# Optimization experiments

Measured on AMD Instinct MI355X. Metric: run time of the kernel, lower is better.

Reference implementation:

```python
import jax, jax.numpy as jnp
import numpy as np
from jax import lax

DIM = 384
HEADS = 8
DIM_HEAD = 64
INNER = HEADS * DIM_HEAD  # 512
K = 3
B, H, W = 8, 56, 56
EPS = 1e-5
SCALE = DIM_HEAD ** -0.5


def _dw_proj(x, w_dw, bn_g, bn_b, bn_m, bn_v, w_pw):
    """DepthWiseConv2d: depthwise kxk conv (groups=C_in) -> BatchNorm (inference) -> 1x1 conv."""
    c_in = x.shape[1]
    y = lax.conv_general_dilated(
        x, w_dw, window_strides=(1, 1), padding='SAME',
        feature_group_count=c_in,
        dimension_numbers=('NCHW', 'OIHW', 'NCHW'))
    inv = bn_g / jnp.sqrt(bn_v + EPS)
    y = y * inv[None, :, None, None] + (bn_b - bn_m * inv)[None, :, None, None]
    # 1x1 conv as einsum over channels
    return jnp.einsum('bchw,oc->bohw', y, w_pw)


def _split_heads(t):
    # b (h d) x y -> (b h) (x y) d
    b, _, hh, ww = t.shape
    t = t.reshape(b, HEADS, DIM_HEAD, hh * ww)
    return t.transpose(0, 1, 3, 2).reshape(b * HEADS, hh * ww, DIM_HEAD)


def setup_inputs() -> dict:
    key = jax.random.key(0)
    ks = jax.random.split(key, 12)
    inp = {
        'x': jax.random.normal(ks[0], (B, DIM, H, W), jnp.float32),
        'wq_dw': jax.random.normal(ks[1], (DIM, 1, K, K), jnp.float32) * 0.1,
        'wq_bn_g': jax.random.normal(ks[2], (DIM,), jnp.float32) * 0.1 + 1.0,
        'wq_bn_b': jax.random.normal(ks[3], (DIM,), jnp.float32) * 0.1,
        'wq_bn_m': jax.random.normal(ks[4], (DIM,), jnp.float32) * 0.1,
        'wq_bn_v': jax.random.uniform(ks[5], (DIM,), jnp.float32, 0.5, 1.5),
        'wq_pw': jax.random.normal(ks[6], (INNER, DIM), jnp.float32) * (DIM ** -0.5),
        'wkv_dw': jax.random.normal(ks[7], (DIM, 1, K, K), jnp.float32) * 0.1,
        'wkv_bn_g': jax.random.normal(ks[8], (DIM,), jnp.float32) * 0.1 + 1.0,
        'wkv_bn_b': jax.random.normal(ks[9], (DIM,), jnp.float32) * 0.1,
        'wkv_bn_m': jax.random.normal(ks[10], (DIM,), jnp.float32) * 0.1,
        'wkv_bn_v': jax.random.uniform(ks[11], (DIM,), jnp.float32, 0.5, 1.5),
    }
    k2 = jax.random.split(jax.random.fold_in(key, 1), 3)
    inp['wkv_pw'] = jax.random.normal(k2[0], (2 * INNER, DIM), jnp.float32) * (DIM ** -0.5)
    inp['wo'] = jax.random.normal(k2[1], (DIM, INNER), jnp.float32) * (INNER ** -0.5)
    inp['bo'] = jax.random.normal(k2[2], (DIM,), jnp.float32) * 0.01
    return inp


def reference(x, wq_dw, wq_bn_g, wq_bn_b, wq_bn_m, wq_bn_v, wq_pw,
              wkv_dw, wkv_bn_g, wkv_bn_b, wkv_bn_m, wkv_bn_v, wkv_pw, wo, bo):
    b, _, hh, ww = x.shape
    q = _dw_proj(x, wq_dw, wq_bn_g, wq_bn_b, wq_bn_m, wq_bn_v, wq_pw)
    kv = _dw_proj(x, wkv_dw, wkv_bn_g, wkv_bn_b, wkv_bn_m, wkv_bn_v, wkv_pw)
    k, v = kv[:, :INNER], kv[:, INNER:]
    q, k, v = _split_heads(q), _split_heads(k), _split_heads(v)  # (b*h, N, d)

    # Original math: M0 = diag((q*k).sum(-1))*s; M1+M2 = s*q@k^T;
    # out = M0.sum()*v + (M1 - M0)@v + M2@v = M0.sum()*v + s*q@(k^T@v) - diag*v
    diag = (q * k).sum(-1) * SCALE              # (bh, N)
    m0_sum = diag.sum()                          # global scalar
    ktv = jnp.einsum('bnd,bne->bde', k, v)       # (bh, d, d) -- O(N d^2)
    out = m0_sum * v + SCALE * jnp.einsum('bnd,bde->bne', q, ktv) - diag[..., None] * v

    # (b h) (x y) d -> b (h d) x y
    out = out.reshape(b, HEADS, hh * ww, DIM_HEAD).transpose(0, 1, 3, 2)
    out = out.reshape(b, INNER, hh, ww)
    # to_out: 1x1 conv with bias (dropout p=0)
    return jnp.einsum('bchw,oc->bohw', out, wo) + bo[None, :, None, None]
```

## Files before the change

kernel.cpp:

```cpp
#include <hip/hip_runtime.h>

typedef unsigned short u16;

#define N_SP   3136
#define BNCOL  25088
#define NDIM   384
#define NINNER 512
#define SCALE_F 0.125f

typedef __attribute__((ext_vector_type(8))) short bf16x8;
typedef __attribute__((ext_vector_type(4))) float f32x4;

#define AS1 __attribute__((address_space(1)))
#define AS3 __attribute__((address_space(3)))

__device__ __forceinline__ float bf2f(u16 u) {
  union { unsigned int i; float f; } v; v.i = ((unsigned int)u) << 16; return v.f;
}
__device__ __forceinline__ u16 f2bf(float f) {
  union { float f; unsigned int i; } v; v.f = f;
  unsigned int r = v.i + 0x7fffu + ((v.i >> 16) & 1u);
  return (u16)(r >> 16);
}

__device__ __forceinline__ void g2l16(const u16* g, u16* l) {
  __builtin_amdgcn_global_load_lds((const AS1 unsigned int*)g,
                                   (AS3 unsigned int*)l, 16, 0, 0);
}

__global__ __launch_bounds__(256) void cvt_kernel(
    const float* __restrict__ a, const float* __restrict__ b, const float* __restrict__ c,
    u16* __restrict__ oa, u16* __restrict__ ob, u16* __restrict__ oc,
    const float* __restrict__ qdw, const float* __restrict__ qg, const float* __restrict__ qb2,
    const float* __restrict__ qm,  const float* __restrict__ qv,
    const float* __restrict__ kdw, const float* __restrict__ kg, const float* __restrict__ kb2,
    const float* __restrict__ km,  const float* __restrict__ kvv,
    float* __restrict__ fused)
{
  int i = blockIdx.x * 256 + threadIdx.x;
  if (i < 196608) oa[i] = f2bf(a[i]);
  ob[i] = f2bf(b[i]);
  if (i < 196608) oc[i] = f2bf(c[i]);
  if (i < NDIM) {
    float invq = qg[i] * rsqrtf(qv[i] + 1e-5f);
    float invk = kg[i] * rsqrtf(kvv[i] + 1e-5f);
    float* f = fused + i * 20;
#pragma unroll
    for (int j = 0; j < 9; ++j) { f[j] = qdw[i*9+j] * invq; f[10+j] = kdw[i*9+j] * invk; }
    f[9]  = qb2[i] - qm[i] * invq;
    f[19] = kb2[i] - km[i] * invk;
  }
}

__global__ __launch_bounds__(256) void dwbn_kernel(
    const float* __restrict__ x, const float* __restrict__ fused,
    u16* __restrict__ yq, u16* __restrict__ ykv)
{
  __shared__ u16 Lq[64][40];
  __shared__ u16 Lk[64][40];
  int tid = threadIdx.x;
  int bb = blockIdx.z, c0 = blockIdx.y * 32, p0 = blockIdx.x * 64;
  int pl = tid & 63;
  int cg = __builtin_amdgcn_readfirstlane(tid >> 6);
  int p = p0 + pl;
  int h = p / 56, w = p - h * 56;
  int roff[3], coff[3];
  float mr[3], mc[3];
#pragma unroll
  for (int d = 0; d < 3; ++d) {
    int r = h + d - 1;
    bool vr = (r >= 0) && (r < 56);
    roff[d] = (vr ? r : h) * 56;
    mr[d] = vr ? 1.f : 0.f;
    int cc = w + d - 1;
    bool vc = (cc >= 0) && (cc < 56);
    coff[d] = vc ? cc : w;
    mc[d] = vc ? 1.f : 0.f;
  }
  float m9[9];
#pragma unroll
  for (int dh = 0; dh < 3; ++dh)
#pragma unroll
    for (int dw = 0; dw < 3; ++dw) m9[dh*3+dw] = mr[dh] * mc[dw];

  __attribute__((aligned(16))) u16 oq[8], ok[8];
#pragma unroll
  for (int i = 0; i < 8; ++i) {
    int c = c0 + cg * 8 + i;
    const float* xp = x + ((size_t)bb * NDIM + c) * N_SP;
    const float* f = fused + c * 20;
    float v[9];
#pragma unroll
    for (int dh = 0; dh < 3; ++dh)
#pragma unroll
      for (int dw = 0; dw < 3; ++dw)
        v[dh*3+dw] = xp[roff[dh] + coff[dw]];
    float sq = f[9], sk = f[19];
#pragma unroll
    for (int j = 0; j < 9; ++j) {
      float xm = v[j] * m9[j];
      sq += xm * f[j];
      sk += xm * f[10+j];
    }
    oq[i] = f2bf(sq); ok[i] = f2bf(sk);
  }
  *(ushort4*)&Lq[pl][cg * 8]     = *(ushort4*)&oq[0];
  *(ushort4*)&Lq[pl][cg * 8 + 4] = *(ushort4*)&oq[4];
  *(ushort4*)&Lk[pl][cg * 8]     = *(ushort4*)&ok[0];
  *(ushort4*)&Lk[pl][cg * 8 + 4] = *(ushort4*)&ok[4];
  __syncthreads();
  int pr = tid >> 2, cc2 = (tid & 3) * 8;
  size_t g = ((size_t)bb * N_SP + p0 + pr) * NDIM + c0 + cc2;
  *(ushort4*)(yq + g)      = *(ushort4*)&Lq[pr][cc2];
  *(ushort4*)(yq + g + 4)  = *(ushort4*)&Lq[pr][cc2 + 4];
  *(ushort4*)(ykv + g)     = *(ushort4*)&Lk[pr][cc2];
  *(ushort4*)(ykv + g + 4) = *(ushort4*)&Lk[pr][cc2 + 4];
}

struct GemmLds {
  union {
    struct { u16 A[128 * 32]; u16 B[128 * 32]; } s;
    u16 T[64 * 132];
  } u;
};

__device__ __forceinline__ void gemm_body(GemmLds& lds, int bid,
    const u16* __restrict__ A, const u16* __restrict__ B, int Kd,
    u16* __restrict__ Cout, int Cstride,
    int mode, const float* __restrict__ bias, float* __restrict__ Out, int Mt, int Nt)
{
  int mt, nt;
  if (Nt == 8) {
    int low = bid & 7;
    nt = (bid >> 3) & 7;
    mt = (bid >> 6) * 8 + low;
    if (mt >= Mt) return;
  } else {
    int r = bid & 7, g = bid >> 3;
    mt = g % Mt; nt = (g / Mt) * 8 + r;
    if (nt >= Nt) return;
  }
  int m0 = mt * 128, n0 = nt * 128;

  int tid = threadIdx.x;
  int lane = tid & 63, wv = tid >> 6;
  int wm = (wv >> 1) * 64, wn = (wv & 1) * 64;
  int srow = lane >> 2;
  int sch = (lane & 3) * 8;
  int arow0 = wv * 32;
  const u16* Ag = A + (size_t)(m0 + arow0 + srow) * Kd + sch;
  const u16* Bg = B + (size_t)(n0 + arow0 + srow) * Kd + sch;
  u16* Al = &lds.u.s.A[arow0 * 32];
  u16* Bl = &lds.u.s.B[arow0 * 32];
  f32x4 acc[4][4];
#pragma unroll
  for (int i = 0; i < 4; ++i)
#pragma unroll
    for (int j = 0; j < 4; ++j) acc[i][j] = (f32x4){0.f, 0.f, 0.f, 0.f};

  int ml = lane & 15, q8 = (lane >> 4) * 8;
  for (int k0 = 0; k0 < Kd; k0 += 32) {
    g2l16(Ag + k0, Al);
    g2l16(Ag + k0 + (size_t)16 * Kd, Al + 16 * 32);
    g2l16(Bg + k0, Bl);
    g2l16(Bg + k0 + (size_t)16 * Kd, Bl + 16 * 32);
    __syncthreads();
    bf16x8 af[4], bfr[4];
#pragma unroll
    for (int i = 0; i < 4; ++i) {
      af[i]  = *(const bf16x8*)&lds.u.s.A[(wm + i * 16 + ml) * 32 + q8];
      bfr[i] = *(const bf16x8*)&lds.u.s.B[(wn + i * 16 + ml) * 32 + q8];
    }
#pragma unroll
    for (int i = 0; i < 4; ++i)
#pragma unroll
      for (int j = 0; j < 4; ++j)
        acc[i][j] = __builtin_amdgcn_mfma_f32_16x16x32_bf16(af[i], bfr[j], acc[i][j], 0, 0, 0);
    __syncthreads();
  }

  if (mode == 0) {
    int q4 = (lane >> 4) * 4;
#pragma unroll
    for (int ph = 0; ph < 2; ++ph) {
      if (ph) __syncthreads();
      if ((wv & 1) == ph) {
#pragma unroll
        for (int i = 0; i < 4; ++i)
#pragma unroll
          for (int j = 0; j < 4; ++j) {
            int nl = j * 16 + ml;
            int m = wm + i * 16 + q4;
            ushort4 o;
            o.x = f2bf(acc[i][j][0]); o.y = f2bf(acc[i][j][1]);
            o.z = f2bf(acc[i][j][2]); o.w = f2bf(acc[i][j][3]);
            *(ushort4*)&lds.u.T[nl * 132 + m] = o;
          }
      }
      __syncthreads();
#pragma unroll
      for (int it = 0; it < 4; ++it) {
        int nl = it * 16 + (tid >> 4);
        int mc = (tid & 15) * 8;
        ushort4 a = *(ushort4*)&lds.u.T[nl * 132 + mc];
        ushort4 b = *(ushort4*)&lds.u.T[nl * 132 + mc + 4];
        u16* gp = Cout + (size_t)(n0 + ph * 64 + nl) * Cstride + m0 + mc;
        *(ushort4*)gp = a;
        *(ushort4*)(gp + 4) = b;
      }
    }
  } else {
    int q4 = (lane >> 4) * 4;
#pragma unroll
    for (int i = 0; i < 4; ++i)
#pragma unroll
      for (int j = 0; j < 4; ++j) {
        int n = n0 + wn + j * 16 + ml;
        int bb = n / N_SP, p = n - bb * N_SP;
#pragma unroll
        for (int rr = 0; rr < 4; ++rr) {
          int m = m0 + wm + i * 16 + q4 + rr;
          Out[((size_t)bb * NDIM + m) * N_SP + p] = acc[i][j][rr] + bias[m];
        }
      }
  }
}

__global__ __launch_bounds__(256) void mfma_gemm(
    const u16* __restrict__ A, const u16* __restrict__ B, int Kd,
    u16* __restrict__ Cout, int Cstride,
    int mode, const float* __restrict__ bias, float* __restrict__ Out, int Mt, int Nt)
{
  __shared__ GemmLds lds;
  gemm_body(lds, blockIdx.x, A, B, Kd, Cout, Cstride, mode, bias, Out, Mt, Nt);
}

__global__ __launch_bounds__(256) void mfma_gemm_qkv(
    const u16* __restrict__ Wq, const u16* __restrict__ yq, u16* __restrict__ Qb,
    const u16* __restrict__ ykv, const u16* __restrict__ Wkv, u16* __restrict__ KVb)
{
  __shared__ GemmLds lds;
  int bid = blockIdx.x;
  if (bid < 800)
    gemm_body(lds, bid, Wq, yq, NDIM, Qb, NINNER, 0, nullptr, nullptr, 4, 196);
  else
    gemm_body(lds, bid - 800, ykv, Wkv, NDIM, KVb, BNCOL, 0, nullptr, nullptr, 196, 8);
}

__global__ __launch_bounds__(256) void diag_ktv_kernel(
    const u16* __restrict__ Q, const u16* __restrict__ KV,
    float* __restrict__ dg, float* __restrict__ m0, float* __restrict__ ktv)
{
  __shared__ float wsum[4];
  int bid = blockIdx.x, tid = threadIdx.x;
  if (bid < 448) {
    int bh = bid / 7, xb = bid - bh * 7;
    int bb = bh >> 3, hh = bh & 7;
    int w = tid >> 6, lane = tid & 63;
    int ml = lane & 15, quad = lane >> 4, q8 = quad * 8;
    size_t colbase = (size_t)bb * N_SP + xb * 448 + q8;
    const u16* Ar = KV + (size_t)(hh * 64 + w * 16 + ml) * BNCOL + colbase;
    const u16* Br = KV + (size_t)(NINNER + hh * 64 + ml) * BNCOL + colbase;
    f32x4 acc[4];
#pragma unroll
    for (int j = 0; j < 4; ++j) acc[j] = (f32x4){0.f, 0.f, 0.f, 0.f};
#pragma unroll
    for (int t = 0; t < 14; ++t) {
      int po = t * 32;
      bf16x8 a = *(const bf16x8*)(Ar + po);
#pragma unroll
      for (int j = 0; j < 4; ++j) {
        bf16x8 b = *(const bf16x8*)(Br + (size_t)j * 16 * BNCOL + po);
        acc[j] = __builtin_amdgcn_mfma_f32_16x16x32_bf16(a, b, acc[j], 0, 0, 0);
      }
    }
    float* kt = ktv + bh * 4096;
#pragma unroll
    for (int j = 0; j < 4; ++j)
#pragma unroll
      for (int r = 0; r < 4; ++r)
        atomicAdd(&kt[(w * 16 + quad * 4 + r) * 64 + j * 16 + ml], acc[j][r]);
  } else {
    int b2 = bid - 448;
    int hh = b2 / 98, xb = b2 - hh * 98;
    int bn = xb * 256 + tid;
    const u16* qrow = Q + (size_t)bn * NINNER + hh * 64;
    const u16* kcol = KV + (size_t)(hh * 64) * BNCOL + bn;
    float s = 0.f;
#pragma unroll
    for (int d0 = 0; d0 < 64; d0 += 8) {
      ushort4 a = *(const ushort4*)(qrow + d0);
      ushort4 b = *(const ushort4*)(qrow + d0 + 4);
      const u16* kp = kcol + (size_t)d0 * BNCOL;
      s += bf2f(a.x) * bf2f(kp[0]);
      s += bf2f(a.y) * bf2f(kp[(size_t)1 * BNCOL]);
      s += bf2f(a.z) * bf2f(kp[(size_t)2 * BNCOL]);
      s += bf2f(a.w) * bf2f(kp[(size_t)3 * BNCOL]);
      s += bf2f(b.x) * bf2f(kp[(size_t)4 * BNCOL]);
      s += bf2f(b.y) * bf2f(kp[(size_t)5 * BNCOL]);
      s += bf2f(b.z) * bf2f(kp[(size_t)6 * BNCOL]);
      s += bf2f(b.w) * bf2f(kp[(size_t)7 * BNCOL]);
    }
    s *= SCALE_F;
    dg[(size_t)hh * BNCOL + bn] = s;
    float r = s;
#pragma unroll
    for (int off = 32; off > 0; off >>= 1) r += __shfl_down(r, off);
    if ((tid & 63) == 0) wsum[tid >> 6] = r;
    __syncthreads();
    if (tid == 0) atomicAdd(m0, wsum[0] + wsum[1] + wsum[2] + wsum[3]);
  }
}

__global__ __launch_bounds__(256) void attn_out_kernel(
    const u16* __restrict__ Q, const u16* __restrict__ KV,
    const float* __restrict__ dg, const float* __restrict__ ktv,
    const float* __restrict__ m0p, u16* __restrict__ OutA)
{
  __shared__ u16 Bt[64][72];
  __shared__ u16 T2[64][72];
  __shared__ float ds2[64];
  int bh = blockIdx.y, bb = bh >> 3, hh = bh & 7;
  int p0 = blockIdx.x * 64;
  int tid = threadIdx.x;
  const float* kt = ktv + bh * 4096;
  for (int l = tid; l < 4096; l += 256) {
    int d = l >> 6, e = l & 63;
    Bt[e][d] = f2bf(kt[l]);
  }
  if (tid < 64) ds2[tid] = dg[(size_t)hh * BNCOL + bb * N_SP + p0 + tid];
  __syncthreads();
  int w = tid >> 6, lane = tid & 63;
  int ml = lane & 15, quad = lane >> 4, q8 = quad * 8;
  const u16* Ar = Q + ((size_t)bb * N_SP + p0 + w * 16 + ml) * NINNER + hh * 64 + q8;
  bf16x8 a0 = *(const bf16x8*)Ar;
  bf16x8 a1 = *(const bf16x8*)(Ar + 32);
  f32x4 acc[4];
#pragma unroll
  for (int j = 0; j < 4; ++j) acc[j] = (f32x4){0.f, 0.f, 0.f, 0.f};
#pragma unroll
  for (int j = 0; j < 4; ++j) {
    bf16x8 b0 = *(const bf16x8*)&Bt[j * 16 + ml][q8];
    bf16x8 b1 = *(const bf16x8*)&Bt[j * 16 + ml][32 + q8];
    acc[j] = __builtin_amdgcn_mfma_f32_16x16x32_bf16(a0, b0, acc[j], 0, 0, 0);
    acc[j] = __builtin_amdgcn_mfma_f32_16x16x32_bf16(a1, b1, acc[j], 0, 0, 0);
  }
  float m0v = *m0p;
  size_t pcol = (size_t)bb * N_SP + p0 + w * 16 + quad * 4;
#pragma unroll
  for (int j = 0; j < 4; ++j) {
    const u16* vr = KV + (size_t)(NINNER + hh * 64 + j * 16 + ml) * BNCOL + pcol;
    ushort4 vv = *(const ushort4*)vr;
    const u16* vp = (const u16*)&vv;
#pragma unroll
    for (int r = 0; r < 4; ++r) {
      float dvm = m0v - ds2[w * 16 + quad * 4 + r];
      float o = SCALE_F * acc[j][r] + dvm * bf2f(vp[r]);
      T2[w * 16 + quad * 4 + r][j * 16 + ml] = f2bf(o);
    }
  }
  __syncthreads();
  int pl = tid >> 2, ec = (tid & 3) * 16;
  u16* gp = OutA + ((size_t)bb * N_SP + p0 + pl) * NINNER + hh * 64 + ec;
  *(ushort4*)gp        = *(ushort4*)&T2[pl][ec];
  *(ushort4*)(gp + 4)  = *(ushort4*)&T2[pl][ec + 4];
  *(ushort4*)(gp + 8)  = *(ushort4*)&T2[pl][ec + 8];
  *(ushort4*)(gp + 12) = *(ushort4*)&T2[pl][ec + 12];
}

extern "C" void kernel_launch(void* const* d_in, const int* in_sizes, int n_in,
                              void* d_out, int out_size, void* d_ws, size_t ws_size,
                              hipStream_t stream)
{
  (void)in_sizes; (void)n_in; (void)out_size; (void)ws_size;
  const float* x      = (const float*)d_in[0];
  const float* wq_dw  = (const float*)d_in[1];
  const float* wq_g   = (const float*)d_in[2];
  const float* wq_b   = (const float*)d_in[3];
  const float* wq_m   = (const float*)d_in[4];
  const float* wq_v   = (const float*)d_in[5];
  const float* wq_pw  = (const float*)d_in[6];
  const float* wkv_dw = (const float*)d_in[7];
  const float* wkv_g  = (const float*)d_in[8];
  const float* wkv_b  = (const float*)d_in[9];
  const float* wkv_m  = (const float*)d_in[10];
  const float* wkv_v  = (const float*)d_in[11];
  const float* wkv_pw = (const float*)d_in[12];
  const float* wo     = (const float*)d_in[13];
  const float* bo     = (const float*)d_in[14];
  float* out = (float*)d_out;

  char* ws = (char*)d_ws;
  size_t off = 0;
  auto alloc = [&](size_t bytes) {
    void* p = ws + off; off = (off + bytes + 255) & ~(size_t)255; return p;
  };
  u16* yq   = (u16*)alloc((size_t)BNCOL * NDIM * 2);
  u16* ykv  = (u16*)alloc((size_t)BNCOL * NDIM * 2);
  u16* Qb   = (u16*)alloc((size_t)BNCOL * NINNER * 2);
  u16* KVb  = (u16*)alloc((size_t)2 * NINNER * BNCOL * 2);
  float* dgb  = (float*)alloc((size_t)BNCOL * 8 * 4);
  float* ktvb = (float*)alloc((size_t)64 * 4096 * 4 + 64);
  u16* Wq  = (u16*)alloc((size_t)NINNER * NDIM * 2);
  u16* Wkv = (u16*)alloc((size_t)2 * NINNER * NDIM * 2);
  u16* Wo  = (u16*)alloc((size_t)NDIM * NINNER * 2);
  float* fused = (float*)alloc((size_t)NDIM * 20 * 4);
  float* m0 = ktvb + 64 * 4096;
  u16* OutA = yq;

  hipMemsetAsync(ktvb, 0, (size_t)64 * 4096 * 4 + 4, stream);

  cvt_kernel<<<1536, 256, 0, stream>>>(wq_pw, wkv_pw, wo, Wq, Wkv, Wo,
                                       wq_dw, wq_g, wq_b, wq_m, wq_v,
                                       wkv_dw, wkv_g, wkv_b, wkv_m, wkv_v, fused);

  dwbn_kernel<<<dim3(49, 12, 8), 256, 0, stream>>>(x, fused, yq, ykv);

  mfma_gemm_qkv<<<dim3(800 + 1600), 256, 0, stream>>>(Wq, yq, Qb, ykv, Wkv, KVb);

  diag_ktv_kernel<<<dim3(448 + 784), 256, 0, stream>>>(Qb, KVb, dgb, m0, ktvb);

  attn_out_kernel<<<dim3(49, 64), 256, 0, stream>>>(Qb, KVb, dgb, ktvb, m0, OutA);

  mfma_gemm<<<dim3(3 * 200), 256, 0, stream>>>(Wo, OutA, NINNER, nullptr, 0, 1, bo, out, 3, 196);
}
```

Measured before the change: 299.0 us.

## Double-buffer GEMM LDS tiles and XOR-swizzle chunks to avoid bank conflicts

The GEMM main loop now uses two LDS stages, so the next K-tile's global-to-LDS copy is issued before the MFMAs on the current tile run. This removes one barrier per iteration and overlaps memory latency with compute. It also XOR-swizzles the 8-element chunk index on both the store and load sides to reduce LDS bank conflicts. The cost is double the LDS footprint for A/B tiles (32KB), which may reduce occupancy.

```diff
diff --git a/kernel.cpp b/kernel.cpp
--- a/kernel.cpp
+++ b/kernel.cpp
@@ -119,7 +119,7 @@
 
 struct GemmLds {
   union {
-    struct { u16 A[128 * 32]; u16 B[128 * 32]; } s;
+    u16 buf[2][2][128 * 32];
     u16 T[64 * 132];
   } u;
 };
@@ -146,37 +146,55 @@
   int lane = tid & 63, wv = tid >> 6;
   int wm = (wv >> 1) * 64, wn = (wv & 1) * 64;
   int srow = lane >> 2;
-  int sch = (lane & 3) * 8;
+  int sch = (((lane & 3) ^ ((srow >> 1) & 3))) * 8;
   int arow0 = wv * 32;
   const u16* Ag = A + (size_t)(m0 + arow0 + srow) * Kd + sch;
   const u16* Bg = B + (size_t)(n0 + arow0 + srow) * Kd + sch;
-  u16* Al = &lds.u.s.A[arow0 * 32];
-  u16* Bl = &lds.u.s.B[arow0 * 32];
+
+  int ml = lane & 15;
+  int ch = (((lane >> 4) ^ ((ml >> 1) & 3))) * 8;
+
   f32x4 acc[4][4];
 #pragma unroll
   for (int i = 0; i < 4; ++i)
 #pragma unroll
     for (int j = 0; j < 4; ++j) acc[i][j] = (f32x4){0.f, 0.f, 0.f, 0.f};
 
-  int ml = lane & 15, q8 = (lane >> 4) * 8;
-  for (int k0 = 0; k0 < Kd; k0 += 32) {
+  const int nT = Kd >> 5;
+
+  auto stage = [&](int t, int s) {
+    int k0 = t * 32;
+    u16* Al = &lds.u.buf[s][0][arow0 * 32];
+    u16* Bl = &lds.u.buf[s][1][arow0 * 32];
     g2l16(Ag + k0, Al);
     g2l16(Ag + k0 + (size_t)16 * Kd, Al + 16 * 32);
     g2l16(Bg + k0, Bl);
     g2l16(Bg + k0 + (size_t)16 * Kd, Bl + 16 * 32);
-    __syncthreads();
+  };
+  auto compute = [&](int s) {
+    const u16* As = lds.u.buf[s][0];
+    const u16* Bs = lds.u.buf[s][1];
     bf16x8 af[4], bfr[4];
 #pragma unroll
     for (int i = 0; i < 4; ++i) {
-      af[i]  = *(const bf16x8*)&lds.u.s.A[(wm + i * 16 + ml) * 32 + q8];
-      bfr[i] = *(const bf16x8*)&lds.u.s.B[(wn + i * 16 + ml) * 32 + q8];
+      af[i]  = *(const bf16x8*)&As[(wm + i * 16 + ml) * 32 + ch];
+      bfr[i] = *(const bf16x8*)&Bs[(wn + i * 16 + ml) * 32 + ch];
     }
 #pragma unroll
     for (int i = 0; i < 4; ++i)
 #pragma unroll
       for (int j = 0; j < 4; ++j)
         acc[i][j] = __builtin_amdgcn_mfma_f32_16x16x32_bf16(af[i], bfr[j], acc[i][j], 0, 0, 0);
+  };
+
+  stage(0, 0);
+  __syncthreads();
+  int cur = 0;
+  for (int t = 0; t < nT; ++t) {
+    if (t + 1 < nT) stage(t + 1, cur ^ 1);
+    compute(cur);
     __syncthreads();
+    cur ^= 1;
   }
 
   if (mode == 0) {
```

After: 277.4 us. -7.2%, faster.

## Load GEMM fragments directly from global into registers with double buffering

Applied to the files above, without the earlier changes.

Replaces the LDS-staged global_load_lds tiles in the MFMA GEMM with direct per-lane global loads of bf16x8 fragments, double-buffered across two K-steps of 32, and removes the per-iteration barriers. It also adds a min-blocks hint of 2 to the launch bounds. The goal is to cut LDS traffic and sync stalls. The cost is that each wave now loads its own fragments without sharing through LDS, so global/L2 traffic doubles and the row-strided loads are less coalesced. Register pressure also rises.

```diff
diff --git a/kernel.cpp b/kernel.cpp
--- a/kernel.cpp
+++ b/kernel.cpp
@@ -21,11 +21,6 @@
   union { float f; unsigned int i; } v; v.f = f;
   unsigned int r = v.i + 0x7fffu + ((v.i >> 16) & 1u);
   return (u16)(r >> 16);
-}
-
-__device__ __forceinline__ void g2l16(const u16* g, u16* l) {
-  __builtin_amdgcn_global_load_lds((const AS1 unsigned int*)g,
-                                   (AS3 unsigned int*)l, 16, 0, 0);
 }
 
 __global__ __launch_bounds__(256) void cvt_kernel(
@@ -117,12 +112,7 @@
   *(ushort4*)(ykv + g + 4) = *(ushort4*)&Lk[pr][cc2 + 4];
 }
 
-struct GemmLds {
-  union {
-    struct { u16 A[128 * 32]; u16 B[128 * 32]; } s;
-    u16 T[64 * 132];
-  } u;
-};
+struct GemmLds { u16 T[64 * 132]; };
 
 __device__ __forceinline__ void gemm_body(GemmLds& lds, int bid,
     const u16* __restrict__ A, const u16* __restrict__ B, int Kd,
@@ -145,38 +135,46 @@
   int tid = threadIdx.x;
   int lane = tid & 63, wv = tid >> 6;
   int wm = (wv >> 1) * 64, wn = (wv & 1) * 64;
-  int srow = lane >> 2;
-  int sch = (lane & 3) * 8;
-  int arow0 = wv * 32;
-  const u16* Ag = A + (size_t)(m0 + arow0 + srow) * Kd + sch;
-  const u16* Bg = B + (size_t)(n0 + arow0 + srow) * Kd + sch;
-  u16* Al = &lds.u.s.A[arow0 * 32];
-  u16* Bl = &lds.u.s.B[arow0 * 32];
+  int ml = lane & 15, q8 = (lane >> 4) * 8;
+
+  const u16* Ar = A + (size_t)(m0 + wm + ml) * Kd + q8;
+  const u16* Br = B + (size_t)(n0 + wn + ml) * Kd + q8;
+
   f32x4 acc[4][4];
 #pragma unroll
   for (int i = 0; i < 4; ++i)
 #pragma unroll
     for (int j = 0; j < 4; ++j) acc[i][j] = (f32x4){0.f, 0.f, 0.f, 0.f};
 
-  int ml = lane & 15, q8 = (lane >> 4) * 8;
-  for (int k0 = 0; k0 < Kd; k0 += 32) {
-    g2l16(Ag + k0, Al);
-    g2l16(Ag + k0 + (size_t)16 * Kd, Al + 16 * 32);
-    g2l16(Bg + k0, Bl);
-    g2l16(Bg + k0 + (size_t)16 * Kd, Bl + 16 * 32);
-    __syncthreads();
-    bf16x8 af[4], bfr[4];
+  bf16x8 a0[4], b0[4], a1[4], b1[4];
+#pragma unroll
+  for (int i = 0; i < 4; ++i) {
+    a0[i] = *(const bf16x8*)(Ar + (size_t)(i * 16) * Kd);
+    b0[i] = *(const bf16x8*)(Br + (size_t)(i * 16) * Kd);
+  }
+  for (int k0 = 0; k0 < Kd; k0 += 64) {
 #pragma unroll
     for (int i = 0; i < 4; ++i) {
-      af[i]  = *(const bf16x8*)&lds.u.s.A[(wm + i * 16 + ml) * 32 + q8];
-      bfr[i] = *(const bf16x8*)&lds.u.s.B[(wn + i * 16 + ml) * 32 + q8];
+      a1[i] = *(const bf16x8*)(Ar + (size_t)(i * 16) * Kd + k0 + 32);
+      b1[i] = *(const bf16x8*)(Br + (size_t)(i * 16) * Kd + k0 + 32);
     }
 #pragma unroll
     for (int i = 0; i < 4; ++i)
 #pragma unroll
       for (int j = 0; j < 4; ++j)
-        acc[i][j] = __builtin_amdgcn_mfma_f32_16x16x32_bf16(af[i], bfr[j], acc[i][j], 0, 0, 0);
-    __syncthreads();
+        acc[i][j] = __builtin_amdgcn_mfma_f32_16x16x32_bf16(a0[i], b0[j], acc[i][j], 0, 0, 0);
+    if (k0 + 64 < Kd) {
+#pragma unroll
+      for (int i = 0; i < 4; ++i) {
+        a0[i] = *(const bf16x8*)(Ar + (size_t)(i * 16) * Kd + k0 + 64);
+        b0[i] = *(const bf16x8*)(Br + (size_t)(i * 16) * Kd + k0 + 64);
+      }
+    }
+#pragma unroll
+    for (int i = 0; i < 4; ++i)
+#pragma unroll
+      for (int j = 0; j < 4; ++j)
+        acc[i][j] = __builtin_amdgcn_mfma_f32_16x16x32_bf16(a1[i], b1[j], acc[i][j], 0, 0, 0);
   }
 
   if (mode == 0) {
@@ -194,7 +192,7 @@
             ushort4 o;
             o.x = f2bf(acc[i][j][0]); o.y = f2bf(acc[i][j][1]);
             o.z = f2bf(acc[i][j][2]); o.w = f2bf(acc[i][j][3]);
-            *(ushort4*)&lds.u.T[nl * 132 + m] = o;
+            *(ushort4*)&lds.T[nl * 132 + m] = o;
           }
       }
       __syncthreads();
@@ -202,8 +200,8 @@
       for (int it = 0; it < 4; ++it) {
         int nl = it * 16 + (tid >> 4);
         int mc = (tid & 15) * 8;
-        ushort4 a = *(ushort4*)&lds.u.T[nl * 132 + mc];
-        ushort4 b = *(ushort4*)&lds.u.T[nl * 132 + mc + 4];
+        ushort4 a = *(ushort4*)&lds.T[nl * 132 + mc];
+        ushort4 b = *(ushort4*)&lds.T[nl * 132 + mc + 4];
         u16* gp = Cout + (size_t)(n0 + ph * 64 + nl) * Cstride + m0 + mc;
         *(ushort4*)gp = a;
         *(ushort4*)(gp + 4) = b;
@@ -226,7 +224,7 @@
   }
 }
 
-__global__ __launch_bounds__(256) void mfma_gemm(
+__global__ __launch_bounds__(256, 2) void mfma_gemm(
     const u16* __restrict__ A, const u16* __restrict__ B, int Kd,
     u16* __restrict__ Cout, int Cstride,
     int mode, const float* __restrict__ bias, float* __restrict__ Out, int Mt, int Nt)
@@ -235,7 +233,7 @@
   gemm_body(lds, blockIdx.x, A, B, Kd, Cout, Cstride, mode, bias, Out, Mt, Nt);
 }
 
-__global__ __launch_bounds__(256) void mfma_gemm_qkv(
+__global__ __launch_bounds__(256, 2) void mfma_gemm_qkv(
     const u16* __restrict__ Wq, const u16* __restrict__ yq, u16* __restrict__ Qb,
     const u16* __restrict__ ykv, const u16* __restrict__ Wkv, u16* __restrict__ KVb)
 {
```

After: 346.0 us. 1.16x slower.
